# Performance work log

Measured on AMD Instinct MI355X. Metric: run time of the kernel, lower is better.

Reference implementation:

```python
import jax, jax.numpy as jnp
import numpy as np
from jax import lax

BN_EPS = 1e-5

def _binarize(t):
    # deterministic sign binarization (sign(0)=0, matching torch.sign)
    return jnp.sign(t)

def setup_inputs() -> dict:
    key = jax.random.key(0)
    k1, k2 = jax.random.split(key)
    N, C, H, W = 16, 128, 128, 128
    x = jax.random.normal(k1, (N, C, H, W), dtype=jnp.float32)
    weight = jax.random.normal(k2, (C, C, 3, 3), dtype=jnp.float32)  # OIHW
    gamma = jnp.ones((C,), dtype=jnp.float32)
    beta = jnp.zeros((C,), dtype=jnp.float32)
    return {"x": x, "weight": weight, "gamma": gamma, "beta": beta}

def reference(x, weight, gamma, beta):
    residual = x
    # binarize activations (C != 3 path) and weights
    bx = _binarize(x)
    bw = _binarize(weight)
    # 3x3 conv, stride 1, padding 1, no bias
    out = lax.conv_general_dilated(
        bx, bw,
        window_strides=(1, 1),
        padding=((1, 1), (1, 1)),
        dimension_numbers=("NCHW", "OIHW", "NCHW"),
    )
    # BatchNorm2d in training mode: batch stats over (N, H, W), biased variance
    mean = jnp.mean(out, axis=(0, 2, 3))
    var = jnp.var(out, axis=(0, 2, 3))
    inv = lax.rsqrt(var + BN_EPS)
    out = (out - mean[None, :, None, None]) * (inv * gamma)[None, :, None, None] + beta[None, :, None, None]
    # Hardtanh
    out = jnp.clip(out, -1.0, 1.0)
    return out + residual
```

## Files before the change

### kernel.cpp

```cpp
#include <hip/hip_runtime.h>
#include <stdint.h>

#define Nn 16
#define Cc 128
#define Hh 128
#define Ww 128
#define HWc (Hh*Ww)
#define NPIX (Nn*Hh*Ww)
#define NHW 262144

typedef int v4i  __attribute__((ext_vector_type(4)));
typedef int v16i __attribute__((ext_vector_type(16)));


__global__ __launch_bounds__(256) void pack_x(const float* __restrict__ x,
                                              char* __restrict__ x8) {
    __shared__ char tile[128 * 132];
    int bid = blockIdx.x;
    int n = bid >> 7, h = bid & 127;
    const float* px = x + (((size_t)n * 128) * 128 + h) * 128;
    int t = threadIdx.x;
    int w = t & 127, ch = t >> 7;
    for (int q = 0; q < 16; ++q) {
        int c = ch * 64 + q * 4;
        uint32_t d = 0;
        #pragma unroll
        for (int j = 0; j < 4; ++j) {
            float v = px[(size_t)(c + j) * HWc + w];
            int8_t s = (v > 0.f) ? 1 : ((v < 0.f) ? -1 : 0);
            d |= (uint32_t)(uint8_t)s << (8 * j);
        }
        *(uint32_t*)(tile + w * 132 + c) = d;
    }
    __syncthreads();
    char* dst = x8 + (size_t)bid * 16384;
    for (int s = 0; s < 4; ++s) {
        int idx = s * 256 + t;
        int ww = idx >> 3, cb = idx & 7;
        const char* src = tile + ww * 132 + cb * 16;
        uint32_t a0 = *(const uint32_t*)(src + 0);
        uint32_t a1 = *(const uint32_t*)(src + 4);
        uint32_t a2 = *(const uint32_t*)(src + 8);
        uint32_t a3 = *(const uint32_t*)(src + 12);
        *(uint4*)(dst + ww * 128 + cb * 16) = make_uint4(a0, a1, a2, a3);
    }
}

__global__ __launch_bounds__(256) void pack_w(const float* __restrict__ wt,
                                              char* __restrict__ wswz) {
    int gid = blockIdx.x * 256 + threadIdx.x;
    if (gid >= 9216) return;
    int lane = gid & 63, grp = gid >> 6;
    int kh = grp & 3, tap = (grp >> 2) % 9, ot = grp / 36;
    int o  = ot * 32 + (lane & 31);
    int cb = kh * 32 + (lane >> 5) * 16;
    uint32_t dw[4];
    #pragma unroll
    for (int di = 0; di < 4; ++di) {
        uint32_t d = 0;
        #pragma unroll
        for (int j = 0; j < 4; ++j) {
            int c = cb + di * 4 + j;
            float v = wt[((size_t)o * 128 + c) * 9 + tap];
            int8_t s = (v > 0.f) ? 1 : ((v < 0.f) ? -1 : 0);
            d |= (uint32_t)(uint8_t)s << (8 * j);
        }
        dw[di] = d;
    }
    *(uint4*)(wswz + (size_t)gid * 16) = make_uint4(dw[0], dw[1], dw[2], dw[3]);
}

__global__ __launch_bounds__(256) void conv_mfma(const char* __restrict__ x8,
                                                 const char* __restrict__ wswz,
                                                 float* __restrict__ out) {
    int bid = blockIdx.x;
    int n = bid >> 7, h = bid & 127;
    int tid = threadIdx.x;
    int lane = tid & 63, wid = tid >> 6;
    int wy = wid >> 1, wx = wid & 1;
    int ln31 = lane & 31, lq = lane >> 5;

    v16i acc[2][2];
    #pragma unroll
    for (int oi = 0; oi < 2; ++oi)
        #pragma unroll
        for (int pi = 0; pi < 2; ++pi)
            #pragma unroll
            for (int r = 0; r < 16; ++r) acc[oi][pi][r] = 0;

    const char* xim = x8 + ((size_t)n * 128) * 16384;
    int w2a = wx * 64 + ln31;
    #pragma unroll
    for (int tap = 0; tap < 9; ++tap) {
        int dh = tap / 3 - 1, dw = tap % 3 - 1;
        int h2 = h + dh;
        bool rowok = (unsigned)h2 < 128u;
        int wa = w2a + dw, wb = wa + 32;
        bool va = rowok && ((unsigned)wa < 128u);
        bool vb = rowok && ((unsigned)wb < 128u);
        const char* prow  = xim + (size_t)h2 * 16384;
        const char* wbase = wswz + (size_t)((wy * 2) * 9 + tap) * 4096;
        #pragma unroll
        for (int kh = 0; kh < 4; ++kh) {
            int co = kh * 32 + lq * 16;
            v4i a0 = *(const v4i*)(wbase + kh * 1024 + lane * 16);
            v4i a1 = *(const v4i*)(wbase + 9 * 4096 + kh * 1024 + lane * 16);
            v4i b0; v4i b1;
            #pragma unroll
            for (int r = 0; r < 4; ++r) { b0[r] = 0; b1[r] = 0; }
            if (va) b0 = *(const v4i*)(prow + (size_t)wa * 128 + co);
            if (vb) b1 = *(const v4i*)(prow + (size_t)wb * 128 + co);
            acc[0][0] = __builtin_amdgcn_mfma_i32_32x32x32_i8(a0, b0, acc[0][0], 0, 0, 0);
            acc[0][1] = __builtin_amdgcn_mfma_i32_32x32x32_i8(a0, b1, acc[0][1], 0, 0, 0);
            acc[1][0] = __builtin_amdgcn_mfma_i32_32x32x32_i8(a1, b0, acc[1][0], 0, 0, 0);
            acc[1][1] = __builtin_amdgcn_mfma_i32_32x32x32_i8(a1, b1, acc[1][1], 0, 0, 0);
        }
    }

    float* po = out + ((size_t)n * 128) * HWc + (size_t)h * 128;
    #pragma unroll
    for (int oi = 0; oi < 2; ++oi)
        #pragma unroll
        for (int pi = 0; pi < 2; ++pi) {
            int wcol = wx * 64 + pi * 32 + ln31;
            #pragma unroll
            for (int r = 0; r < 16; ++r) {
                int orow = wy * 64 + oi * 32 + (r & 3) + 8 * (r >> 2) + 4 * lq;
                po[(size_t)orow * HWc + wcol] = (float)acc[oi][pi][r];
            }
        }
}

__global__ __launch_bounds__(256) void stats_kernel(const float* __restrict__ conv,
                                                    unsigned long long* __restrict__ stats) {
    int b = blockIdx.x;
    int c = b & 127, n = b >> 7;
    const float4* p = (const float4*)(conv + (size_t)(n * Cc + c) * HWc);
    int sum = 0, sq = 0;
    for (int i = threadIdx.x; i < HWc / 4; i += 256) {
        float4 v = p[i];
        int a = (int)v.x, d = (int)v.y, e = (int)v.z, f = (int)v.w;
        sum += a + d + e + f;
        sq  += a * a + d * d + e * e + f * f;
    }
    #pragma unroll
    for (int off = 32; off > 0; off >>= 1) {
        sum += __shfl_down(sum, off);
        sq  += __shfl_down(sq, off);
    }
    __shared__ int wsum[4], wsq[4];
    int wave = threadIdx.x >> 6, lane = threadIdx.x & 63;
    if (lane == 0) { wsum[wave] = sum; wsq[wave] = sq; }
    __syncthreads();
    if (threadIdx.x == 0) {
        int S = 0, Q = 0;
        #pragma unroll
        for (int i = 0; i < 4; ++i) { S += wsum[i]; Q += wsq[i]; }
        atomicAdd(&stats[c],       (unsigned long long)(long long)S);
        atomicAdd(&stats[128 + c], (unsigned long long)(long long)Q);
    }
}

__global__ __launch_bounds__(256) void apply_kernel(float* __restrict__ out,
                                                    const float* __restrict__ x,
                                                    const unsigned long long* __restrict__ stats,
                                                    const float* __restrict__ gamma,
                                                    const float* __restrict__ beta) {
    int b = blockIdx.x;
    int c = b & 127, n = b >> 7;
    size_t basei = (size_t)(n * Cc + c) * HWc;
    long long S = (long long)stats[c];
    long long Q = (long long)stats[128 + c];
    double m   = (double)S / (double)NHW;
    double var = (double)Q / (double)NHW - m * m;
    float inv   = (float)(1.0 / sqrt(var + 1e-5));
    float scale = inv * gamma[c];
    float shift = beta[c] - (float)m * scale;

    float4* po = (float4*)(out + basei);
    const float4* px = (const float4*)(x + basei);
    for (int i = threadIdx.x; i < HWc / 4; i += 256) {
        float4 v = po[i];
        float4 r = px[i];
        v.x = fminf(fmaxf(v.x * scale + shift, -1.0f), 1.0f) + r.x;
        v.y = fminf(fmaxf(v.y * scale + shift, -1.0f), 1.0f) + r.y;
        v.z = fminf(fmaxf(v.z * scale + shift, -1.0f), 1.0f) + r.z;
        v.w = fminf(fmaxf(v.w * scale + shift, -1.0f), 1.0f) + r.w;
        po[i] = v;
    }
}

extern "C" void kernel_launch(void* const* d_in, const int* in_sizes, int n_in,
                              void* d_out, int out_size, void* d_ws, size_t ws_size,
                              hipStream_t stream) {
    const float* x     = (const float*)d_in[0];
    const float* wt    = (const float*)d_in[1];
    const float* gamma = (const float*)d_in[2];
    const float* beta  = (const float*)d_in[3];
    float* out = (float*)d_out;

    char* ws = (char*)d_ws;
    unsigned long long* stats = (unsigned long long*)ws;
    char* wswz = ws + 4096;
    char* x8   = ws + 262144;

    hipMemsetAsync(stats, 0, 2048, stream);
    pack_x<<<Nn * Hh, 256, 0, stream>>>(x, x8);
    pack_w<<<36, 256, 0, stream>>>(wt, wswz);
    conv_mfma<<<Nn * Hh, 256, 0, stream>>>(x8, wswz, out);
    stats_kernel<<<Nn * Cc, 256, 0, stream>>>(out, stats);
    apply_kernel<<<Nn * Cc, 256, 0, stream>>>(out, x, stats, gamma, beta);
}
```

Measured before the change: 401.5 us.

## Pad packed activations, stage conv rows in LDS, store int16 intermediate

Packed int8 activations now carry zero halo rows and columns with a padded pixel stride. Each conv block loads its three input rows into LDS through global_load_lds, which removes the per-tap bounds checks and the repeated global gathers. The conv result is written as int16 to a workspace buffer when one is large enough. This halves the intermediate traffic through the stats and apply passes, at the cost of more LDS per block and a fallback float path when the workspace is too small.

```diff
diff --git a/kernel.cpp b/kernel.cpp
--- a/kernel.cpp
+++ b/kernel.cpp
@@ -6,20 +6,40 @@
 #define Hh 128
 #define Ww 128
 #define HWc (Hh*Ww)
-#define NPIX (Nn*Hh*Ww)
 #define NHW 262144
+
+#define PIXB 132
+#define ROWP 17408
+#define NROW 130
 
 typedef int v4i  __attribute__((ext_vector_type(4)));
 typedef int v16i __attribute__((ext_vector_type(16)));
 
+typedef __attribute__((address_space(3))) unsigned int lds_uint;
+typedef __attribute__((address_space(1))) const unsigned int glob_uint;
+
+__device__ __forceinline__ void gload_lds16(const void* g, void* l) {
+    __builtin_amdgcn_global_load_lds((glob_uint*)g, (lds_uint*)l, 16, 0, 0);
+}
 
 __global__ __launch_bounds__(256) void pack_x(const float* __restrict__ x,
                                               char* __restrict__ x8) {
-    __shared__ char tile[128 * 132];
     int bid = blockIdx.x;
-    int n = bid >> 7, h = bid & 127;
-    const float* px = x + (((size_t)n * 128) * 128 + h) * 128;
+    int n = bid / NROW, r = bid % NROW;
+    char* row = x8 + (size_t)bid * ROWP;
     int t = threadIdx.x;
+
+    if (r == 0 || r == NROW - 1) {
+        for (int i = t; i < ROWP / 16; i += 256)
+            ((uint4*)row)[i] = make_uint4(0, 0, 0, 0);
+        return;
+    }
+    int h = r - 1;
+    if (t < 33)                ((uint32_t*)row)[t] = 0;
+    else if (t >= 64 && t < 97) ((uint32_t*)(row + 129 * PIXB))[t - 64] = 0;
+
+    __shared__ char tile[128 * PIXB];
+    const float* px = x + (((size_t)n * Cc) * Hh + h) * Ww;
     int w = t & 127, ch = t >> 7;
     for (int q = 0; q < 16; ++q) {
         int c = ch * 64 + q * 4;
@@ -30,19 +50,15 @@
             int8_t s = (v > 0.f) ? 1 : ((v < 0.f) ? -1 : 0);
             d |= (uint32_t)(uint8_t)s << (8 * j);
         }
-        *(uint32_t*)(tile + w * 132 + c) = d;
+        *(uint32_t*)(tile + w * PIXB + c) = d;
     }
     __syncthreads();
-    char* dst = x8 + (size_t)bid * 16384;
     for (int s = 0; s < 4; ++s) {
         int idx = s * 256 + t;
         int ww = idx >> 3, cb = idx & 7;
-        const char* src = tile + ww * 132 + cb * 16;
-        uint32_t a0 = *(const uint32_t*)(src + 0);
-        uint32_t a1 = *(const uint32_t*)(src + 4);
-        uint32_t a2 = *(const uint32_t*)(src + 8);
-        uint32_t a3 = *(const uint32_t*)(src + 12);
-        *(uint4*)(dst + ww * 128 + cb * 16) = make_uint4(a0, a1, a2, a3);
+        const uint32_t* src = (const uint32_t*)(tile + ww * PIXB + cb * 16);
+        uint32_t* dst = (uint32_t*)(row + (1 + ww) * PIXB + cb * 16);
+        dst[0] = src[0]; dst[1] = src[1]; dst[2] = src[2]; dst[3] = src[3];
     }
 }
 
@@ -54,29 +70,39 @@
     int kh = grp & 3, tap = (grp >> 2) % 9, ot = grp / 36;
     int o  = ot * 32 + (lane & 31);
     int cb = kh * 32 + (lane >> 5) * 16;
-    uint32_t dw[4];
+    uint32_t dw4[4];
     #pragma unroll
     for (int di = 0; di < 4; ++di) {
         uint32_t d = 0;
         #pragma unroll
         for (int j = 0; j < 4; ++j) {
             int c = cb + di * 4 + j;
-            float v = wt[((size_t)o * 128 + c) * 9 + tap];
+            float v = wt[((size_t)o * Cc + c) * 9 + tap];
             int8_t s = (v > 0.f) ? 1 : ((v < 0.f) ? -1 : 0);
             d |= (uint32_t)(uint8_t)s << (8 * j);
         }
-        dw[di] = d;
-    }
-    *(uint4*)(wswz + (size_t)gid * 16) = make_uint4(dw[0], dw[1], dw[2], dw[3]);
-}
-
-__global__ __launch_bounds__(256) void conv_mfma(const char* __restrict__ x8,
-                                                 const char* __restrict__ wswz,
-                                                 float* __restrict__ out) {
+        dw4[di] = d;
+    }
+    *(uint4*)(wswz + (size_t)gid * 16) = make_uint4(dw4[0], dw4[1], dw4[2], dw4[3]);
+}
+
+template <typename OutT>
+__global__ __launch_bounds__(256) void conv_mfma2(const char* __restrict__ x8,
+                                                  const char* __restrict__ wswz,
+                                                  OutT* __restrict__ out) {
+    __shared__ char lds[3 * ROWP];
     int bid = blockIdx.x;
     int n = bid >> 7, h = bid & 127;
-    int tid = threadIdx.x;
-    int lane = tid & 63, wid = tid >> 6;
+    int tid = threadIdx.x, lane = tid & 63, wid = tid >> 6;
+
+    const char* gbase = x8 + ((size_t)n * NROW + h) * ROWP;
+    for (int task = wid; task < 51; task += 4) {
+        int rr = task / 17, ck = task % 17;
+        gload_lds16(gbase + (size_t)rr * ROWP + ck * 1024 + lane * 16,
+                    lds + rr * ROWP + ck * 1024);
+    }
+    __syncthreads();
+
     int wy = wid >> 1, wx = wid & 1;
     int ln31 = lane & 31, lq = lane >> 5;
 
@@ -86,30 +112,23 @@
         #pragma unroll
         for (int pi = 0; pi < 2; ++pi)
             #pragma unroll
-            for (int r = 0; r < 16; ++r) acc[oi][pi][r] = 0;
-
-    const char* xim = x8 + ((size_t)n * 128) * 16384;
-    int w2a = wx * 64 + ln31;
+            for (int r2 = 0; r2 < 16; ++r2) acc[oi][pi][r2] = 0;
+
+    const char* wb0 = wswz + (size_t)(wy * 2 * 9) * 4096 + lane * 16;
+    const char* lb  = lds + (1 + wx * 64 + ln31) * PIXB + lq * 16;
+
     #pragma unroll
     for (int tap = 0; tap < 9; ++tap) {
-        int dh = tap / 3 - 1, dw = tap % 3 - 1;
-        int h2 = h + dh;
-        bool rowok = (unsigned)h2 < 128u;
-        int wa = w2a + dw, wb = wa + 32;
-        bool va = rowok && ((unsigned)wa < 128u);
-        bool vb = rowok && ((unsigned)wb < 128u);
-        const char* prow  = xim + (size_t)h2 * 16384;
-        const char* wbase = wswz + (size_t)((wy * 2) * 9 + tap) * 4096;
+        int rr = tap / 3, dw = tap % 3 - 1;
         #pragma unroll
         for (int kh = 0; kh < 4; ++kh) {
-            int co = kh * 32 + lq * 16;
-            v4i a0 = *(const v4i*)(wbase + kh * 1024 + lane * 16);
-            v4i a1 = *(const v4i*)(wbase + 9 * 4096 + kh * 1024 + lane * 16);
-            v4i b0; v4i b1;
+            v4i a0 = *(const v4i*)(wb0 + (tap * 4 + kh) * 1024);
+            v4i a1 = *(const v4i*)(wb0 + (36 + tap * 4 + kh) * 1024);
+            const uint32_t* p0 = (const uint32_t*)(lb + rr * ROWP + dw * PIXB + kh * 32);
+            const uint32_t* p1 = p0 + (32 * PIXB) / 4;
+            v4i b0, b1;
             #pragma unroll
-            for (int r = 0; r < 4; ++r) { b0[r] = 0; b1[r] = 0; }
-            if (va) b0 = *(const v4i*)(prow + (size_t)wa * 128 + co);
-            if (vb) b1 = *(const v4i*)(prow + (size_t)wb * 128 + co);
+            for (int j = 0; j < 4; ++j) { b0[j] = (int)p0[j]; b1[j] = (int)p1[j]; }
             acc[0][0] = __builtin_amdgcn_mfma_i32_32x32x32_i8(a0, b0, acc[0][0], 0, 0, 0);
             acc[0][1] = __builtin_amdgcn_mfma_i32_32x32x32_i8(a0, b1, acc[0][1], 0, 0, 0);
             acc[1][0] = __builtin_amdgcn_mfma_i32_32x32x32_i8(a1, b0, acc[1][0], 0, 0, 0);
@@ -117,22 +136,56 @@
         }
     }
 
-    float* po = out + ((size_t)n * 128) * HWc + (size_t)h * 128;
+    OutT* po = out + ((size_t)n * Cc) * HWc + (size_t)h * Ww;
     #pragma unroll
     for (int oi = 0; oi < 2; ++oi)
         #pragma unroll
         for (int pi = 0; pi < 2; ++pi) {
             int wcol = wx * 64 + pi * 32 + ln31;
             #pragma unroll
-            for (int r = 0; r < 16; ++r) {
-                int orow = wy * 64 + oi * 32 + (r & 3) + 8 * (r >> 2) + 4 * lq;
-                po[(size_t)orow * HWc + wcol] = (float)acc[oi][pi][r];
+            for (int r2 = 0; r2 < 16; ++r2) {
+                int orow = wy * 64 + oi * 32 + (r2 & 3) + 8 * (r2 >> 2) + 4 * lq;
+                po[(size_t)orow * HWc + wcol] = (OutT)acc[oi][pi][r2];
             }
         }
 }
 
-__global__ __launch_bounds__(256) void stats_kernel(const float* __restrict__ conv,
-                                                    unsigned long long* __restrict__ stats) {
+__global__ __launch_bounds__(256) void stats16(const short* __restrict__ conv,
+                                               unsigned long long* __restrict__ stats) {
+    int b = blockIdx.x;
+    int c = b & 127, n = b >> 7;
+    const uint4* p = (const uint4*)(conv + (size_t)(n * Cc + c) * HWc);
+    int sum = 0, sq = 0;
+    for (int i = threadIdx.x; i < HWc / 8; i += 256) {
+        uint4 v = p[i];
+        uint32_t ua[4] = {v.x, v.y, v.z, v.w};
+        #pragma unroll
+        for (int j = 0; j < 4; ++j) {
+            int s0 = (short)(ua[j] & 0xffff), s1 = (short)(ua[j] >> 16);
+            sum += s0 + s1;
+            sq  += s0 * s0 + s1 * s1;
+        }
+    }
+    #pragma unroll
+    for (int off = 32; off > 0; off >>= 1) {
+        sum += __shfl_down(sum, off);
+        sq  += __shfl_down(sq, off);
+    }
+    __shared__ int wsum[4], wsq[4];
+    int wave = threadIdx.x >> 6, lane = threadIdx.x & 63;
+    if (lane == 0) { wsum[wave] = sum; wsq[wave] = sq; }
+    __syncthreads();
+    if (threadIdx.x == 0) {
+        long long S = 0, Q = 0;
+        #pragma unroll
+        for (int i = 0; i < 4; ++i) { S += wsum[i]; Q += wsq[i]; }
+        atomicAdd(&stats[c],       (unsigned long long)S);
+        atomicAdd(&stats[128 + c], (unsigned long long)Q);
+    }
+}
+
+__global__ __launch_bounds__(256) void statsf(const float* __restrict__ conv,
+                                              unsigned long long* __restrict__ stats) {
     int b = blockIdx.x;
     int c = b & 127, n = b >> 7;
     const float4* p = (const float4*)(conv + (size_t)(n * Cc + c) * HWc);
@@ -153,29 +206,71 @@
     if (lane == 0) { wsum[wave] = sum; wsq[wave] = sq; }
     __syncthreads();
     if (threadIdx.x == 0) {
-        int S = 0, Q = 0;
+        long long S = 0, Q = 0;
         #pragma unroll
         for (int i = 0; i < 4; ++i) { S += wsum[i]; Q += wsq[i]; }
-        atomicAdd(&stats[c],       (unsigned long long)(long long)S);
-        atomicAdd(&stats[128 + c], (unsigned long long)(long long)Q);
-    }
-}
-
-__global__ __launch_bounds__(256) void apply_kernel(float* __restrict__ out,
-                                                    const float* __restrict__ x,
-                                                    const unsigned long long* __restrict__ stats,
-                                                    const float* __restrict__ gamma,
-                                                    const float* __restrict__ beta) {
-    int b = blockIdx.x;
-    int c = b & 127, n = b >> 7;
-    size_t basei = (size_t)(n * Cc + c) * HWc;
+        atomicAdd(&stats[c],       (unsigned long long)S);
+        atomicAdd(&stats[128 + c], (unsigned long long)Q);
+    }
+}
+
+__device__ __forceinline__ void bn_coef(const unsigned long long* stats,
+                                        const float* gamma, const float* beta,
+                                        int c, float& scale, float& shift) {
     long long S = (long long)stats[c];
     long long Q = (long long)stats[128 + c];
     double m   = (double)S / (double)NHW;
     double var = (double)Q / (double)NHW - m * m;
-    float inv   = (float)(1.0 / sqrt(var + 1e-5));
-    float scale = inv * gamma[c];
-    float shift = beta[c] - (float)m * scale;
+    float inv  = (float)(1.0 / sqrt(var + 1e-5));
+    scale = inv * gamma[c];
+    shift = beta[c] - (float)m * scale;
+}
+
+__global__ __launch_bounds__(256) void apply16(float* __restrict__ out,
+                                               const short* __restrict__ conv,
+                                               const float* __restrict__ x,
+                                               const unsigned long long* __restrict__ stats,
+                                               const float* __restrict__ gamma,
+                                               const float* __restrict__ beta) {
+    int b = blockIdx.x;
+    int c = b & 127, n = b >> 7;
+    size_t basei = (size_t)(n * Cc + c) * HWc;
+    float scale, shift;
+    bn_coef(stats, gamma, beta, c, scale, shift);
+
+    const uint4*  pc = (const uint4*)(conv + basei);
+    const float4* px = (const float4*)(x + basei);
+    float4*       po = (float4*)(out + basei);
+    for (int i = threadIdx.x; i < HWc / 8; i += 256) {
+        uint4 v = pc[i];
+        uint32_t ua[4] = {v.x, v.y, v.z, v.w};
+        #pragma unroll
+        for (int half = 0; half < 2; ++half) {
+            float4 r = px[i * 2 + half];
+            float4 o;
+            float c0 = (float)(short)(ua[half * 2]     & 0xffff);
+            float c1 = (float)(short)(ua[half * 2]     >> 16);
+            float c2 = (float)(short)(ua[half * 2 + 1] & 0xffff);
+            float c3 = (float)(short)(ua[half * 2 + 1] >> 16);
+            o.x = fminf(fmaxf(c0 * scale + shift, -1.0f), 1.0f) + r.x;
+            o.y = fminf(fmaxf(c1 * scale + shift, -1.0f), 1.0f) + r.y;
+            o.z = fminf(fmaxf(c2 * scale + shift, -1.0f), 1.0f) + r.z;
+            o.w = fminf(fmaxf(c3 * scale + shift, -1.0f), 1.0f) + r.w;
+            po[i * 2 + half] = o;
+        }
+    }
+}
+
+__global__ __launch_bounds__(256) void applyf(float* __restrict__ out,
+                                              const float* __restrict__ x,
+                                              const unsigned long long* __restrict__ stats,
+                                              const float* __restrict__ gamma,
+                                              const float* __restrict__ beta) {
+    int b = blockIdx.x;
+    int c = b & 127, n = b >> 7;
+    size_t basei = (size_t)(n * Cc + c) * HWc;
+    float scale, shift;
+    bn_coef(stats, gamma, beta, c, scale, shift);
 
     float4* po = (float4*)(out + basei);
     const float4* px = (const float4*)(x + basei);
@@ -203,11 +298,21 @@
     unsigned long long* stats = (unsigned long long*)ws;
     char* wswz = ws + 4096;
     char* x8   = ws + 262144;
+    const size_t x8_bytes = (size_t)Nn * NROW * ROWP;
+    short* conv16 = (short*)(ws + 262144 + x8_bytes);
+    const size_t need16 = 262144 + x8_bytes + (size_t)NHW * Cc * 2;
 
     hipMemsetAsync(stats, 0, 2048, stream);
-    pack_x<<<Nn * Hh, 256, 0, stream>>>(x, x8);
+    pack_x<<<Nn * NROW, 256, 0, stream>>>(x, x8);
     pack_w<<<36, 256, 0, stream>>>(wt, wswz);
-    conv_mfma<<<Nn * Hh, 256, 0, stream>>>(x8, wswz, out);
-    stats_kernel<<<Nn * Cc, 256, 0, stream>>>(out, stats);
-    apply_kernel<<<Nn * Cc, 256, 0, stream>>>(out, x, stats, gamma, beta);
-}
+
+    if (ws_size >= need16) {
+        conv_mfma2<short><<<Nn * Hh, 256, 0, stream>>>(x8, wswz, conv16);
+        stats16<<<Nn * Cc, 256, 0, stream>>>(conv16, stats);
+        apply16<<<Nn * Cc, 256, 0, stream>>>(out, conv16, x, stats, gamma, beta);
+    } else {
+        conv_mfma2<float><<<Nn * Hh, 256, 0, stream>>>(x8, wswz, out);
+        statsf<<<Nn * Cc, 256, 0, stream>>>(out, stats);
+        applyf<<<Nn * Cc, 256, 0, stream>>>(out, x, stats, gamma, beta);
+    }
+}
```

Measured after the change: 362.9 us. 1.11x faster.
